# Kernel optimization log

Measured on AMD Instinct MI355X. Metric: run time of the kernel, lower is better.

## Reference

```python
import jax, jax.numpy as jnp
import numpy as np

B, T, NIN, H = 256, 100, 64, 1024


def _lstm_cell(x, h, c, Wih, Whh, bih, bhh):
    # torch.nn.LSTMCell: gates = x@Wih^T + bih + h@Whh^T + bhh, order (i, f, g, o)
    gates = x @ Wih.T + bih + h @ Whh.T + bhh  # [B, 4H]
    i, f, g, o = jnp.split(gates, 4, axis=-1)
    i = jax.nn.sigmoid(i)
    f = jax.nn.sigmoid(f)
    g = jnp.tanh(g)
    o = jax.nn.sigmoid(o)
    c_new = f * c + i * g
    h_new = o * jnp.tanh(c_new)
    return h_new, c_new


def setup_inputs() -> dict:
    key = jax.random.key(0)
    ks = jax.random.split(key, 17)
    s_in = 1.0 / np.sqrt(H)
    d = {"x": jax.random.normal(ks[0], (B, T, NIN), dtype=jnp.float32)}
    dims_in = [NIN, H, H, H]
    ki = 1
    for layer in range(1, 5):
        din = dims_in[layer - 1]
        d[f"Wih{layer}"] = jax.random.normal(ks[ki], (4 * H, din), dtype=jnp.float32) * s_in; ki += 1
        d[f"Whh{layer}"] = jax.random.normal(ks[ki], (4 * H, H), dtype=jnp.float32) * s_in; ki += 1
        d[f"bih{layer}"] = jax.random.normal(ks[ki], (4 * H,), dtype=jnp.float32) * s_in; ki += 1
        d[f"bhh{layer}"] = jax.random.normal(ks[ki], (4 * H,), dtype=jnp.float32) * s_in; ki += 1
        ks = jax.random.split(ks[-1], 17)
        ki = 0
    return d


def reference(x, Wih1, Whh1, bih1, bhh1, Wih2, Whh2, bih2, bhh2,
              Wih3, Whh3, bih3, bhh3, Wih4, Whh4, bih4, bhh4):
    batch = x.shape[0]
    params = ((Wih1, Whh1, bih1, bhh1), (Wih2, Whh2, bih2, bhh2),
              (Wih3, Whh3, bih3, bhh3), (Wih4, Whh4, bih4, bhh4))
    zeros = jnp.zeros((batch, H), dtype=x.dtype)
    init = tuple((zeros, zeros) for _ in range(4))

    def step(carry, xt):
        new_carry = []
        inp = xt
        for (h, c), (Wih, Whh, bih, bhh) in zip(carry, params):
            h, c = _lstm_cell(inp, h, c, Wih, Whh, bih, bhh)
            new_carry.append((h, c))
            inp = h
        return tuple(new_carry), inp  # top-layer h

    xs = jnp.swapaxes(x, 0, 1)  # [T, B, NIN]
    carry, hs = jax.lax.scan(step, init, xs)
    out = jnp.swapaxes(hs, 0, 1)  # [B, T, H]
    c4 = carry[3][1]
    return out, c4
```

## Files before the change

### kernel.cpp

```cpp
#include <hip/hip_runtime.h>
#include <hip/hip_bf16.h>

typedef __hip_bfloat16 bf16;
typedef unsigned short u16;
typedef unsigned int u32;
typedef __attribute__((ext_vector_type(8))) short bf16x8;
typedef __attribute__((ext_vector_type(4))) float f32x4;

#define BATCH 256
#define TLEN 100
#define HDIM 1024
#define G4 4096
#define HSTRIDE (BATCH * HDIM)
#define OUT_HT (BATCH * TLEN * HDIM)

#define WS_W0 0u
#define WS_W1 8912896u
#define WS_W2 25690112u
#define WS_W3 42467328u
#define WS_BIAS 59244544u
#define WS_XT 59310080u
#define WS_H 62586880u
#define WS_BAR (WS_H + 4194304u)

__device__ __forceinline__ float sigm(float x) { return 1.0f / (1.0f + __expf(-x)); }
__device__ __forceinline__ float tanh_(float x) { return 2.0f / (1.0f + __expf(-2.0f * x)) - 1.0f; }

__device__ __forceinline__ void gl_lds16(const void* g, void* l) {
  __builtin_amdgcn_global_load_lds((const __attribute__((address_space(1))) u32*)g,
                                   (__attribute__((address_space(3))) u32*)l, 16, 0, 0);
}

__device__ __forceinline__ void gbar(u32* arrive, u32* release, u32 epoch, int tid) {
  __syncthreads();
  if (tid == 0) {
    u32 old = __hip_atomic_fetch_add(arrive, 1u, __ATOMIC_ACQ_REL, __HIP_MEMORY_SCOPE_AGENT);
    if (old == 255u) {
      __hip_atomic_store(arrive, 0u, __ATOMIC_RELAXED, __HIP_MEMORY_SCOPE_AGENT);
      __hip_atomic_store(release, epoch, __ATOMIC_RELEASE, __HIP_MEMORY_SCOPE_AGENT);
    } else {
      while (__hip_atomic_load(release, __ATOMIC_RELAXED, __HIP_MEMORY_SCOPE_AGENT) < epoch)
        __builtin_amdgcn_s_sleep(2);
      __builtin_amdgcn_fence(__ATOMIC_ACQUIRE, "agent");
    }
  }
  __syncthreads();
}


__global__ void pack_w(const float* __restrict__ wih, const float* __restrict__ whh,
                       bf16* __restrict__ dst, int K, int din) {
  int i = blockIdx.x * 256 + threadIdx.x;
  int total4 = (G4 * K) >> 2;
  if (i >= total4) return;
  int e = i << 2;
  int row = e / K;
  int k = e - row * K;
#pragma unroll
  for (int j = 0; j < 4; ++j) {
    int kk = k + j;
    float v = (kk < din) ? wih[row * din + kk] : whh[row * HDIM + (kk - din)];
    dst[e + j] = __float2bfloat16(v);
  }
}

__global__ void pack_bias(const float* __restrict__ a, const float* __restrict__ b,
                          float* __restrict__ dst) {
  int i = blockIdx.x * 256 + threadIdx.x;
  if (i < G4) dst[i] = a[i] + b[i];
}

__global__ void pack_x(const float* __restrict__ x, bf16* __restrict__ xT) {
  int i = blockIdx.x * 256 + threadIdx.x;
  if (i >= TLEN * BATCH * 64) return;
  int k = i & 63;
  int b = (i >> 6) & 255;
  int t = i >> 14;
  xT[i] = __float2bfloat16(x[(b * TLEN + t) * 64 + k]);
}


__global__ void __launch_bounds__(512, 2)
lstm_main(const bf16* __restrict__ Wall, const float* __restrict__ biasc,
          const bf16* __restrict__ xT, bf16* __restrict__ hbuf,
          float* __restrict__ out, u32* __restrict__ barr) {
  __shared__ __align__(16) u16 smem[65536];
  float* Gs = (float*)smem;

  const int tid = threadIdx.x;
  const int lane = tid & 63;
  const int wave = tid >> 6;
  const int wg = blockIdx.x;
  const int layer = wg >> 6;
  const int sub = wg & 63;
  const int b0 = (sub >> 5) * 128;
  const int h0 = (sub & 31) * 32;

  const int K = (layer == 0) ? 1088 : 2048;
  const int NC = K >> 6;
  const bf16* Wl = Wall + ((layer == 0) ? 0 : (4456448 + (size_t)(layer - 1) * 8388608));

  const int nn = tid & 31;
  float bias_r[4];
#pragma unroll
  for (int g = 0; g < 4; ++g) bias_r[g] = biasc[layer * G4 + g * HDIM + h0 + nn];

  const int r0 = (tid >> 5) * 8;
  float cst[8];
#pragma unroll
  for (int k = 0; k < 8; ++k) cst[k] = 0.0f;

  const int srow = lane >> 3;
  const int sk = (((lane & 7) ^ srow) << 4) >> 1;
  int arow[2], wrow[2];
#pragma unroll
  for (int q = 0; q < 2; ++q) {
    int j = (wave * 2 + q) * 8 + srow;
    arow[q] = b0 + j;
    wrow[q] = ((j >> 5) << 10) + h0 + (j & 31);
  }

  const int mb = (wave & 3) * 32;
  const int nbase = (wave >> 2) * 64;
  const int lrow = lane & 15;
  const int lcb0 = (lane >> 4) << 4;
  const int lswz = (lane & 7) << 4;

  u32* bar_arrive = barr;
  u32* bar_release = barr + 32;

  for (int s = 0; s < TLEN + 3; ++s) {
    const int t = s - layer;
    if (t >= 0 && t < TLEN) {
      const bf16* hin = hbuf + ((layer == 0) ? 0 : ((size_t)((layer - 1) * 2 + (t & 1)) * HSTRIDE));
      const bf16* hprev = hbuf + (size_t)(layer * 2 + ((t + 1) & 1)) * HSTRIDE;
      const bf16* xrow = xT + (size_t)t * (BATCH * 64);

      f32x4 acc[2][4];
#pragma unroll
      for (int mt = 0; mt < 2; ++mt)
#pragma unroll
        for (int nt = 0; nt < 4; ++nt) acc[mt][nt] = (f32x4)(0.0f);

      auto stage = [&](int c, int buf) {
#pragma unroll
        for (int q = 0; q < 2; ++q) {
          const bf16* src;
          if (layer == 0) {
            src = (c == 0) ? (xrow + arow[q] * 64 + sk)
                           : (hprev + arow[q] * HDIM + (c - 1) * 64 + sk);
          } else {
            src = (c < 16) ? (hin + arow[q] * HDIM + c * 64 + sk)
                           : (hprev + arow[q] * HDIM + (c - 16) * 64 + sk);
          }
          gl_lds16(src, smem + buf * 8192 + (wave * 2 + q) * 512);
        }
#pragma unroll
        for (int q = 0; q < 2; ++q) {
          const bf16* src = Wl + (size_t)wrow[q] * K + c * 64 + sk;
          gl_lds16(src, smem + 32768 + buf * 8192 + (wave * 2 + q) * 512);
        }
      };

      stage(0, 0);
      stage(1, 1);
      stage(2, 2);

      for (int c = 0; c < NC; ++c) {
        const int buf = c & 3;
        if (c + 3 < NC) stage(c + 3, (c + 3) & 3);

        const int rem = NC - 1 - c;
        if (rem >= 3)      asm volatile("s_waitcnt vmcnt(12)" ::: "memory");
        else if (rem == 2) asm volatile("s_waitcnt vmcnt(8)" ::: "memory");
        else if (rem == 1) asm volatile("s_waitcnt vmcnt(4)" ::: "memory");
        else               asm volatile("s_waitcnt vmcnt(0)" ::: "memory");
        __builtin_amdgcn_s_barrier();

        const char* Abuf = (const char*)smem + buf * 16384;
        const char* Bbuf = (const char*)smem + 65536 + buf * 16384;
        bf16x8 a[2][2], b[2][4];
#pragma unroll
        for (int ks = 0; ks < 2; ++ks) {
#pragma unroll
          for (int mt = 0; mt < 2; ++mt) {
            int row = mb + mt * 16 + lrow;
            a[ks][mt] = *(const bf16x8*)(Abuf + row * 128 + ((ks * 64 + lcb0) ^ lswz));
          }
#pragma unroll
          for (int nt = 0; nt < 4; ++nt) {
            int j = nbase + nt * 16 + lrow;
            b[ks][nt] = *(const bf16x8*)(Bbuf + j * 128 + ((ks * 64 + lcb0) ^ lswz));
          }
        }
        __builtin_amdgcn_s_barrier();

#pragma unroll
        for (int ks = 0; ks < 2; ++ks)
#pragma unroll
          for (int mt = 0; mt < 2; ++mt)
#pragma unroll
            for (int nt = 0; nt < 4; ++nt)
              acc[mt][nt] = __builtin_amdgcn_mfma_f32_16x16x32_bf16(a[ks][mt], b[ks][nt], acc[mt][nt], 0, 0, 0);
      }

      __syncthreads();

#pragma unroll
      for (int mt = 0; mt < 2; ++mt)
#pragma unroll
        for (int nt = 0; nt < 4; ++nt) {
          int row = mb + mt * 16 + (lane >> 4) * 4;
          int col = nbase + nt * 16 + (lane & 15);
#pragma unroll
          for (int r = 0; r < 4; ++r) Gs[(row + r) * 132 + col] = acc[mt][nt][r];
        }
      __syncthreads();

      bf16* hout = hbuf + (size_t)(layer * 2 + (t & 1)) * HSTRIDE;
#pragma unroll
      for (int k = 0; k < 8; ++k) {
        int r = r0 + k;
        float gi = Gs[r * 132 + nn] + bias_r[0];
        float gf = Gs[r * 132 + 32 + nn] + bias_r[1];
        float gg = Gs[r * 132 + 64 + nn] + bias_r[2];
        float go = Gs[r * 132 + 96 + nn] + bias_r[3];
        float iv = sigm(gi), fv = sigm(gf), gv = tanh_(gg), ov = sigm(go);
        float cv = fv * cst[k] + iv * gv;
        cst[k] = cv;
        float hv = ov * tanh_(cv);
        hout[(b0 + r) * HDIM + h0 + nn] = __float2bfloat16(hv);
        if (layer == 3) {
          out[((size_t)(b0 + r) * TLEN + t) * HDIM + h0 + nn] = hv;
          if (t == TLEN - 1) out[OUT_HT + (size_t)(b0 + r) * HDIM + h0 + nn] = cv;
        }
      }
    }
    if (s < TLEN + 2) gbar(bar_arrive, bar_release, (u32)(s + 1), tid);
  }
}


extern "C" void kernel_launch(void* const* d_in, const int* in_sizes, int n_in,
                              void* d_out, int out_size, void* d_ws, size_t ws_size,
                              hipStream_t stream) {
  const float* x = (const float*)d_in[0];
  const float* Wih[4] = {(const float*)d_in[1], (const float*)d_in[5],
                         (const float*)d_in[9], (const float*)d_in[13]};
  const float* Whh[4] = {(const float*)d_in[2], (const float*)d_in[6],
                         (const float*)d_in[10], (const float*)d_in[14]};
  const float* bih[4] = {(const float*)d_in[3], (const float*)d_in[7],
                         (const float*)d_in[11], (const float*)d_in[15]};
  const float* bhh[4] = {(const float*)d_in[4], (const float*)d_in[8],
                         (const float*)d_in[12], (const float*)d_in[16]};

  char* ws = (char*)d_ws;
  bf16* Wall = (bf16*)(ws + WS_W0);
  float* biasc = (float*)(ws + WS_BIAS);
  bf16* xT = (bf16*)(ws + WS_XT);
  bf16* hbuf = (bf16*)(ws + WS_H);
  u32* barr = (u32*)(ws + WS_BAR);
  float* out = (float*)d_out;

  for (int l = 0; l < 4; ++l) {
    int K = (l == 0) ? 1088 : 2048;
    int din = (l == 0) ? 64 : 1024;
    bf16* dst = Wall + ((l == 0) ? 0 : (4456448 + (size_t)(l - 1) * 8388608));
    int total4 = (4096 * K) >> 2;
    pack_w<<<(total4 + 255) / 256, 256, 0, stream>>>(Wih[l], Whh[l], dst, K, din);
    pack_bias<<<16, 256, 0, stream>>>(bih[l], bhh[l], biasc + l * 4096);
  }
  pack_x<<<(TLEN * BATCH * 64 + 255) / 256, 256, 0, stream>>>(x, xT);
  hipMemsetAsync(hbuf, 0, 4194304u + 256u, stream);

  void* args[] = {(void*)&Wall, (void*)&biasc, (void*)&xT, (void*)&hbuf, (void*)&out, (void*)&barr};
  hipLaunchCooperativeKernel((void*)lstm_main, dim3(256), dim3(512), args, 0, stream);
}
```

Before: 3.556 ms.

## Pre-tile and pre-swizzle weights and hidden state into contiguous chunks; drop per-chunk barrier

```diff
diff --git a/kernel.cpp b/kernel.cpp
--- a/kernel.cpp
+++ b/kernel.cpp
@@ -11,13 +11,9 @@
 #define TLEN 100
 #define HDIM 1024
 #define G4 4096
-#define HSTRIDE (BATCH * HDIM)
 #define OUT_HT (BATCH * TLEN * HDIM)
 
-#define WS_W0 0u
-#define WS_W1 8912896u
-#define WS_W2 25690112u
-#define WS_W3 42467328u
+#define WS_WP 0u
 #define WS_BIAS 59244544u
 #define WS_XT 59310080u
 #define WS_H 62586880u
@@ -49,19 +45,18 @@
 
 
 __global__ void pack_w(const float* __restrict__ wih, const float* __restrict__ whh,
-                       bf16* __restrict__ dst, int K, int din) {
+                       bf16* __restrict__ dst, int NC, int din) {
   int i = blockIdx.x * 256 + threadIdx.x;
-  int total4 = (G4 * K) >> 2;
-  if (i >= total4) return;
-  int e = i << 2;
-  int row = e / K;
-  int k = e - row * K;
-#pragma unroll
-  for (int j = 0; j < 4; ++j) {
-    int kk = k + j;
-    float v = (kk < din) ? wih[row * din + kk] : whh[row * HDIM + (kk - din)];
-    dst[e + j] = __float2bfloat16(v);
-  }
+  if (i >= 32 * NC * 128 * 64) return;
+  int k6 = i & 63;
+  int r = (i >> 6) & 127;
+  int jc = i >> 13;
+  int c = jc % NC;
+  int j = jc / NC;
+  int grow = ((r >> 5) << 10) + j * 32 + (r & 31);
+  int k = c * 64 + k6;
+  float v = (k < din) ? wih[grow * din + k] : whh[(grow << 10) + (k - din)];
+  dst[(jc << 13) + (r << 6) + (k6 ^ ((r & 7) << 3))] = __float2bfloat16(v);
 }
 
 __global__ void pack_bias(const float* __restrict__ a, const float* __restrict__ b,
@@ -76,15 +71,15 @@
   int k = i & 63;
   int b = (i >> 6) & 255;
   int t = i >> 14;
-  xT[i] = __float2bfloat16(x[(b * TLEN + t) * 64 + k]);
+  xT[(t << 14) + (b << 6) + (k ^ ((b & 7) << 3))] = __float2bfloat16(x[(b * TLEN + t) * 64 + k]);
 }
 
 
 __global__ void __launch_bounds__(512, 2)
-lstm_main(const bf16* __restrict__ Wall, const float* __restrict__ biasc,
-          const bf16* __restrict__ xT, bf16* __restrict__ hbuf,
+lstm_main(const u16* __restrict__ Wp, const float* __restrict__ biasc,
+          const u16* __restrict__ xT, u16* __restrict__ hbuf,
           float* __restrict__ out, u32* __restrict__ barr) {
-  __shared__ __align__(16) u16 smem[65536];
+  __shared__ __align__(16) u16 smem[73728];
   float* Gs = (float*)smem;
 
   const int tid = threadIdx.x;
@@ -96,9 +91,10 @@
   const int b0 = (sub >> 5) * 128;
   const int h0 = (sub & 31) * 32;
 
-  const int K = (layer == 0) ? 1088 : 2048;
-  const int NC = K >> 6;
-  const bf16* Wl = Wall + ((layer == 0) ? 0 : (4456448 + (size_t)(layer - 1) * 8388608));
+  const int NC = (layer == 0) ? 17 : 32;
+  const int T0 = (layer == 0) ? 1 : 16;
+  const u16* Wsl = Wp + ((layer == 0) ? 0u : (4456448u + (u32)(layer - 1) * 8388608u))
+                 + (u32)(sub & 31) * (u32)NC * 8192u;
 
   const int nn = tid & 31;
   float bias_r[4];
@@ -110,15 +106,8 @@
 #pragma unroll
   for (int k = 0; k < 8; ++k) cst[k] = 0.0f;
 
-  const int srow = lane >> 3;
-  const int sk = (((lane & 7) ^ srow) << 4) >> 1;
-  int arow[2], wrow[2];
-#pragma unroll
-  for (int q = 0; q < 2; ++q) {
-    int j = (wave * 2 + q) * 8 + srow;
-    arow[q] = b0 + j;
-    wrow[q] = ((j >> 5) << 10) + h0 + (j & 31);
-  }
+  const int opu0 = (wave * 2) * 512 + lane * 8;
+  const int opu1 = opu0 + 512;
 
   const int mb = (wave & 3) * 32;
   const int nbase = (wave >> 2) * 64;
@@ -132,9 +121,10 @@
   for (int s = 0; s < TLEN + 3; ++s) {
     const int t = s - layer;
     if (t >= 0 && t < TLEN) {
-      const bf16* hin = hbuf + ((layer == 0) ? 0 : ((size_t)((layer - 1) * 2 + (t & 1)) * HSTRIDE));
-      const bf16* hprev = hbuf + (size_t)(layer * 2 + ((t + 1) & 1)) * HSTRIDE;
-      const bf16* xrow = xT + (size_t)t * (BATCH * 64);
+      const u16* aBase0 = ((layer == 0) ? (xT + (u32)t * 16384u)
+                                        : (hbuf + (u32)((layer - 1) * 2 + (t & 1)) * 262144u))
+                        + b0 * 64;
+      const u16* aBase1 = hbuf + (u32)(layer * 2 + ((t + 1) & 1)) * 262144u + b0 * 64;
 
       f32x4 acc[2][4];
 #pragma unroll
@@ -142,43 +132,37 @@
 #pragma unroll
         for (int nt = 0; nt < 4; ++nt) acc[mt][nt] = (f32x4)(0.0f);
 
-      auto stage = [&](int c, int buf) {
-#pragma unroll
-        for (int q = 0; q < 2; ++q) {
-          const bf16* src;
-          if (layer == 0) {
-            src = (c == 0) ? (xrow + arow[q] * 64 + sk)
-                           : (hprev + arow[q] * HDIM + (c - 1) * 64 + sk);
-          } else {
-            src = (c < 16) ? (hin + arow[q] * HDIM + c * 64 + sk)
-                           : (hprev + arow[q] * HDIM + (c - 16) * 64 + sk);
-          }
-          gl_lds16(src, smem + buf * 8192 + (wave * 2 + q) * 512);
-        }
-#pragma unroll
-        for (int q = 0; q < 2; ++q) {
-          const bf16* src = Wl + (size_t)wrow[q] * K + c * 64 + sk;
-          gl_lds16(src, smem + 32768 + buf * 8192 + (wave * 2 + q) * 512);
-        }
+      auto issueA = [&](int c, int slot) {
+        const u16* src = (c < T0) ? (aBase0 + c * 16384) : (aBase1 + (c - T0) * 16384);
+        gl_lds16(src + opu0, smem + slot * 8192 + (wave * 2) * 512);
+        gl_lds16(src + opu1, smem + slot * 8192 + (wave * 2 + 1) * 512);
       };
-
-      stage(0, 0);
-      stage(1, 1);
-      stage(2, 2);
-
+      auto issueB = [&](int c, int slot) {
+        const u16* src = Wsl + c * 8192;
+        gl_lds16(src + opu0, smem + 32768 + slot * 8192 + (wave * 2) * 512);
+        gl_lds16(src + opu1, smem + 32768 + slot * 8192 + (wave * 2 + 1) * 512);
+      };
+
+      issueB(0, 0);
+      issueA(0, 0);
+      issueB(1, 1);
+      issueA(1, 1);
+      issueB(2, 2);
+
+      int iar = 0, ibr = 0, iaw = 2, ibw = 3;
       for (int c = 0; c < NC; ++c) {
-        const int buf = c & 3;
-        if (c + 3 < NC) stage(c + 3, (c + 3) & 3);
-
         const int rem = NC - 1 - c;
-        if (rem >= 3)      asm volatile("s_waitcnt vmcnt(12)" ::: "memory");
+        if (rem >= 2) issueA(c + 2, iaw);
+        if (rem >= 3) issueB(c + 3, ibw);
+
+        if (rem >= 3)      asm volatile("s_waitcnt vmcnt(10)" ::: "memory");
         else if (rem == 2) asm volatile("s_waitcnt vmcnt(8)" ::: "memory");
         else if (rem == 1) asm volatile("s_waitcnt vmcnt(4)" ::: "memory");
         else               asm volatile("s_waitcnt vmcnt(0)" ::: "memory");
         __builtin_amdgcn_s_barrier();
 
-        const char* Abuf = (const char*)smem + buf * 16384;
-        const char* Bbuf = (const char*)smem + 65536 + buf * 16384;
+        const char* Abuf = (const char*)smem + iar * 16384;
+        const char* Bbuf = (const char*)smem + 65536 + ibr * 16384;
         bf16x8 a[2][2], b[2][4];
 #pragma unroll
         for (int ks = 0; ks < 2; ++ks) {
@@ -193,8 +177,6 @@
             b[ks][nt] = *(const bf16x8*)(Bbuf + j * 128 + ((ks * 64 + lcb0) ^ lswz));
           }
         }
-        __builtin_amdgcn_s_barrier();
-
 #pragma unroll
         for (int ks = 0; ks < 2; ++ks)
 #pragma unroll
@@ -202,6 +184,11 @@
 #pragma unroll
             for (int nt = 0; nt < 4; ++nt)
               acc[mt][nt] = __builtin_amdgcn_mfma_f32_16x16x32_bf16(a[ks][mt], b[ks][nt], acc[mt][nt], 0, 0, 0);
+
+        iar = (iar + 1) & 3;
+        iaw = (iaw + 1) & 3;
+        ibr = (ibr == 4) ? 0 : ibr + 1;
+        ibw = (ibw == 4) ? 0 : ibw + 1;
       }
 
       __syncthreads();
@@ -217,7 +204,10 @@
         }
       __syncthreads();
 
-      bf16* hout = hbuf + (size_t)(layer * 2 + (t & 1)) * HSTRIDE;
+      u16* outSlot = hbuf + (u32)(layer * 2 + (t & 1)) * 262144u;
+      const int hcol = h0 + nn;
+      const int j2 = hcol >> 6;
+      const int colin = hcol & 63;
 #pragma unroll
       for (int k = 0; k < 8; ++k) {
         int r = r0 + k;
@@ -229,10 +219,12 @@
         float cv = fv * cst[k] + iv * gv;
         cst[k] = cv;
         float hv = ov * tanh_(cv);
-        hout[(b0 + r) * HDIM + h0 + nn] = __float2bfloat16(hv);
+        int b = b0 + r;
+        bf16 hb = __float2bfloat16(hv);
+        outSlot[j2 * 16384 + b * 64 + (colin ^ ((b & 7) << 3))] = *(u16*)&hb;
         if (layer == 3) {
-          out[((size_t)(b0 + r) * TLEN + t) * HDIM + h0 + nn] = hv;
-          if (t == TLEN - 1) out[OUT_HT + (size_t)(b0 + r) * HDIM + h0 + nn] = cv;
+          out[((size_t)b * TLEN + t) * HDIM + hcol] = hv;
+          if (t == TLEN - 1) out[OUT_HT + (size_t)b * HDIM + hcol] = cv;
         }
       }
     }
@@ -255,24 +247,24 @@
                          (const float*)d_in[12], (const float*)d_in[16]};
 
   char* ws = (char*)d_ws;
-  bf16* Wall = (bf16*)(ws + WS_W0);
+  bf16* Wp = (bf16*)(ws + WS_WP);
   float* biasc = (float*)(ws + WS_BIAS);
   bf16* xT = (bf16*)(ws + WS_XT);
-  bf16* hbuf = (bf16*)(ws + WS_H);
+  u16* hbuf = (u16*)(ws + WS_H);
   u32* barr = (u32*)(ws + WS_BAR);
   float* out = (float*)d_out;
 
   for (int l = 0; l < 4; ++l) {
-    int K = (l == 0) ? 1088 : 2048;
+    int NC = (l == 0) ? 17 : 32;
     int din = (l == 0) ? 64 : 1024;
-    bf16* dst = Wall + ((l == 0) ? 0 : (4456448 + (size_t)(l - 1) * 8388608));
-    int total4 = (4096 * K) >> 2;
-    pack_w<<<(total4 + 255) / 256, 256, 0, stream>>>(Wih[l], Whh[l], dst, K, din);
+    bf16* dst = Wp + ((l == 0) ? 0 : (4456448 + (size_t)(l - 1) * 8388608));
+    int total = 32 * NC * 128 * 64;
+    pack_w<<<(total + 255) / 256, 256, 0, stream>>>(Wih[l], Whh[l], dst, NC, din);
     pack_bias<<<16, 256, 0, stream>>>(bih[l], bhh[l], biasc + l * 4096);
   }
   pack_x<<<(TLEN * BATCH * 64 + 255) / 256, 256, 0, stream>>>(x, xT);
-  hipMemsetAsync(hbuf, 0, 4194304u + 256u, stream);
-
-  void* args[] = {(void*)&Wall, (void*)&biasc, (void*)&xT, (void*)&hbuf, (void*)&out, (void*)&barr};
+  hipMemsetAsync(ws + WS_H, 0, 4194304u + 256u, stream);
+
+  void* args[] = {(void*)&Wp, (void*)&biasc, (void*)&xT, (void*)&hbuf, (void*)&out, (void*)&barr};
   hipLaunchCooperativeKernel((void*)lstm_main, dim3(256), dim3(512), args, 0, stream);
 }
```

Result: faster. 3.309 ms (-6.9%).
